# Kernel tuning notes

Hardware: AMD Instinct MI355X
Metric: run time of the kernel (lower is better)

Reference implementation:

```python
import jax, jax.numpy as jnp
import numpy as np

B, C, H, W = 16, 2048, 14, 14
D = 8192  # output_dim


def setup_inputs() -> dict:
    key = jax.random.key(0)
    k1, k2, k3, k4, k5 = jax.random.split(key, 5)
    x = jax.random.normal(k1, (B, C, H, W), dtype=jnp.float32)
    h1 = jax.random.randint(k2, (C,), 0, D, dtype=jnp.int32)
    h2 = jax.random.randint(k3, (C,), 0, D, dtype=jnp.int32)
    s1 = jax.random.randint(k4, (C,), 0, 2, dtype=jnp.int32)
    s2 = jax.random.randint(k5, (C,), 0, 2, dtype=jnp.int32)
    return {"x": x, "h1": h1, "h2": h2, "s1": s1, "s2": s2}


def _count_sketch(x_flat, h, sign, out_dim):
    # x_flat: (B, C, HW); h: (C,) hash buckets; sign: (C,) in {-1,+1}
    xs = x_flat * sign[None, :, None]
    sketch = jnp.zeros((x_flat.shape[0], out_dim, x_flat.shape[2]), dtype=x_flat.dtype)
    return sketch.at[:, h, :].add(xs)  # scatter-add over channel -> bucket


def reference(x, h1, h2, s1, s2):
    b, c, hgt, wid = x.shape
    x_flat = x.reshape(b, c, hgt * wid).astype(jnp.float32)
    sg1 = (2 * s1 - 1).astype(jnp.float32)
    sg2 = (2 * s2 - 1).astype(jnp.float32)
    sketch1 = _count_sketch(x_flat, h1, sg1, D)  # (B, D, HW)
    sketch2 = _count_sketch(x_flat, h2, sg2, D)
    fft1 = jnp.fft.fft(sketch1, axis=1)
    fft2 = jnp.fft.fft(sketch2, axis=1)
    cbp = jnp.fft.ifft(fft1 * fft2, axis=1).real  # circular conv per location
    cbp = cbp.sum(axis=-1)  # sum-pool over HW -> (B, D)
    cbp = jnp.sign(cbp) * jnp.sqrt(jnp.abs(cbp) + 1e-5)  # signed sqrt
    norm = jnp.maximum(jnp.linalg.norm(cbp, axis=1, keepdims=True), 1e-12)
    cbp = cbp / norm  # L2 normalize (matches F.normalize eps=1e-12)
    return cbp.astype(x.dtype)
```

## Files before the change

### kernel.cpp

```cpp
#include <hip/hip_runtime.h>
#include <hip/hip_bf16.h>
#include <math.h>

#define FFT_N 8192
#define HWN 196
#define CCH 2048
#define BATCH 16
#define PBLK 28
#define PPER 7

__device__ __forceinline__ int kof(int j) {
    return ((j >> 11) & 3) | (((j >> 9) & 3) << 2) | (((j >> 7) & 3) << 4) |
           (((j >> 5) & 3) << 6) | (((j >> 3) & 3) << 8) | (((j >> 1) & 3) << 10) |
           ((j & 1) << 12);
}
__device__ __forceinline__ int pof(int k) {
    return ((k & 3) << 11) | (((k >> 2) & 3) << 9) | (((k >> 4) & 3) << 7) |
           (((k >> 6) & 3) << 5) | (((k >> 8) & 3) << 3) | (((k >> 10) & 3) << 1) |
           ((k >> 12) & 1);
}

#define TW_TOTAL 1706

__device__ __forceinline__ float2 cmul(float2 a, float2 b) {
    return make_float2(a.x * b.x - a.y * b.y, a.x * b.y + a.y * b.x);
}

template <int Q4, int OFF>
__device__ __forceinline__ void pass4(float2* z, const float2* T, int tid) {
#pragma unroll
    for (int it = 0; it < FFT_N / 4 / 1024; ++it) {
        int u = tid + 1024 * it;
        int o = u & (Q4 - 1);
        int base = ((u & ~(Q4 - 1)) << 2) | o;
        float2 a = z[base], b = z[base + Q4], c = z[base + 2 * Q4], d = z[base + 3 * Q4];
        float t0r = a.x + c.x, t0i = a.y + c.y, t1r = a.x - c.x, t1i = a.y - c.y;
        float t2r = b.x + d.x, t2i = b.y + d.y, t3r = b.x - d.x, t3i = b.y - d.y;
        float2 u0 = make_float2(t0r + t2r, t0i + t2i);
        float2 u2 = make_float2(t0r - t2r, t0i - t2i);
        float2 u1 = make_float2(t1r + t3i, t1i - t3r);
        float2 u3 = make_float2(t1r - t3i, t1i + t3r);
        float2 w1;
        if constexpr (Q4 == 2048) {
            w1 = T[o & 1023];
            if (o & 1024) {
                const float r = 0.70710678118654752f;
                w1 = make_float2(r * (w1.x + w1.y), r * (w1.y - w1.x));
            }
        } else {
            w1 = T[OFF + o];
        }
        float2 w2 = make_float2(w1.x * w1.x - w1.y * w1.y, 2.f * w1.x * w1.y);
        float2 w3 = cmul(w1, w2);
        z[base] = u0;
        z[base + Q4] = cmul(u1, w1);
        z[base + 2 * Q4] = cmul(u2, w2);
        z[base + 3 * Q4] = cmul(u3, w3);
    }
    __syncthreads();
}

__device__ __forceinline__ void fft8192(float2* z, const float2* T, int tid) {
    pass4<2048, 0>(z, T, tid);
    pass4<512, 1024>(z, T, tid);
    pass4<128, 1536>(z, T, tid);
    pass4<32, 1664>(z, T, tid);
    pass4<8, 1696>(z, T, tid);
    pass4<2, 1704>(z, T, tid);
#pragma unroll
    for (int it = 0; it < 4; ++it) {
        int u = tid + 1024 * it;
        int i0 = 2 * u, i1 = 2 * u + 1;
        float2 a = z[i0], b = z[i1];
        z[i0] = make_float2(a.x + b.x, a.y + b.y);
        z[i1] = make_float2(a.x - b.x, a.y - b.y);
    }
    __syncthreads();
}

__device__ __forceinline__ void build_tables(float2* T, int tid) {
    const float w0 = -7.66990393942820573e-4f;
    {
        float s, c; sincosf(w0 * (float)tid, &s, &c); T[tid] = make_float2(c, s);
    }
    if (tid < 512) {
        float s, c; sincosf(w0 * (float)(tid * 4), &s, &c); T[1024 + tid] = make_float2(c, s);
    }
    if (tid < 128) {
        float s, c; sincosf(w0 * (float)(tid * 16), &s, &c); T[1536 + tid] = make_float2(c, s);
    }
    if (tid < 32) {
        float s, c; sincosf(w0 * (float)(tid * 64), &s, &c); T[1664 + tid] = make_float2(c, s);
    }
    if (tid < 8) {
        float s, c; sincosf(w0 * (float)(tid * 256), &s, &c); T[1696 + tid] = make_float2(c, s);
    }
    if (tid < 2) {
        float s, c; sincosf(w0 * (float)(tid * 1024), &s, &c); T[1704 + tid] = make_float2(c, s);
    }
}

__global__ __launch_bounds__(1024) void cbp_fwd(
    const float* __restrict__ x, const int* __restrict__ h1,
    const int* __restrict__ h2, const int* __restrict__ s1,
    const int* __restrict__ s2, float2* __restrict__ acc) {
    __shared__ float2 z[FFT_N];
    __shared__ float2 T[TW_TOTAL];
    int tid = threadIdx.x;
    int b = blockIdx.x / PBLK;
    int pb = blockIdx.x % PBLK;

    build_tables(T, tid);

    int c0 = tid, c1 = tid + 1024;
    int h1a = h1[c0], h2a = h2[c0], h1b = h1[c1], h2b = h2[c1];
    float g1a = (float)(2 * s1[c0] - 1), g2a = (float)(2 * s2[c0] - 1);
    float g1b = (float)(2 * s1[c1] - 1), g2b = (float)(2 * s2[c1] - 1);

    float accR[8], accI[8];
#pragma unroll
    for (int s = 0; s < 8; s++) { accR[s] = 0.f; accI[s] = 0.f; }

    const float* xa = x + (size_t)b * CCH * HWN + (size_t)c0 * HWN + pb * PPER;
    const float* xc = x + (size_t)b * CCH * HWN + (size_t)c1 * HWN + pb * PPER;

    float v0 = xa[0];
    float v1 = xc[0];

    for (int ip = 0; ip < PPER; ++ip) {
        float nv0 = 0.f, nv1 = 0.f;
        if (ip + 1 < PPER) { nv0 = xa[ip + 1]; nv1 = xc[ip + 1]; }

#pragma unroll
        for (int s = 0; s < 8; s++) z[tid + 1024 * s] = make_float2(0.f, 0.f);
        __syncthreads();
        atomicAdd(&z[h1a].x, g1a * v0);
        atomicAdd(&z[h2a].y, g2a * v0);
        atomicAdd(&z[h1b].x, g1b * v1);
        atomicAdd(&z[h2b].y, g2b * v1);
        __syncthreads();

        fft8192(z, T, tid);

#pragma unroll
        for (int s = 0; s < 8; s++) {
            int j = tid + 1024 * s;
            int k = kof(j);
            int m = (FFT_N - k) & (FFT_N - 1);
            int j2 = pof(m);
            float2 a = z[j], bz = z[j2];
            float Dr = (a.x * a.x - a.y * a.y) - (bz.x * bz.x - bz.y * bz.y);
            float Di = 2.f * (a.x * a.y + bz.x * bz.y);
            accR[s] += 0.25f * Di;
            accI[s] -= 0.25f * Dr;
        }
        __syncthreads();
        v0 = nv0; v1 = nv1;
    }

    float2* ab = acc + (size_t)b * FFT_N;
#pragma unroll
    for (int s = 0; s < 8; s++) {
        int j = tid + 1024 * s;
        atomicAdd(&ab[j].x, accR[s]);
        atomicAdd(&ab[j].y, accI[s]);
    }
}

__global__ __launch_bounds__(1024) void cbp_inv(
    const float2* __restrict__ acc, float* __restrict__ out) {
    __shared__ float2 z[FFT_N];
    __shared__ float2 T[TW_TOTAL];
    __shared__ float red[20];
    int tid = threadIdx.x;
    int b = blockIdx.x;

    build_tables(T, tid);

    const float2* ab = acc + (size_t)b * FFT_N;
#pragma unroll
    for (int s = 0; s < 8; s++) {
        int j = tid + 1024 * s;
        float2 v = ab[j];
        z[kof(j)] = make_float2(v.x, -v.y);
    }
    __syncthreads();

    fft8192(z, T, tid);

    float sv[8];
    float ss = 0.f;
#pragma unroll
    for (int s = 0; s < 8; s++) {
        int j = tid + 1024 * s;
        float v = z[j].x * (1.f / (float)FFT_N);
        float r = copysignf(sqrtf(fabsf(v) + 1e-5f), v);
        sv[s] = r;
        ss += r * r;
    }
#pragma unroll
    for (int m = 32; m >= 1; m >>= 1) ss += __shfl_xor(ss, m);
    int wave = tid >> 6, lane = tid & 63;
    if (lane == 0) red[wave] = ss;
    __syncthreads();
    if (tid == 0) {
        float tot = 0.f;
        for (int w = 0; w < 16; w++) tot += red[w];
        red[16] = fmaxf(sqrtf(tot), 1e-12f);
    }
    __syncthreads();
    float inv = 1.f / red[16];
    float* ob = out + (size_t)b * FFT_N;
#pragma unroll
    for (int s = 0; s < 8; s++) {
        int j = tid + 1024 * s;
        ob[kof(j)] = sv[s] * inv;
    }
}

extern "C" void kernel_launch(void* const* d_in, const int* in_sizes, int n_in,
                              void* d_out, int out_size, void* d_ws, size_t ws_size,
                              hipStream_t stream) {
    const float* x = (const float*)d_in[0];
    const int* h1 = (const int*)d_in[1];
    const int* h2 = (const int*)d_in[2];
    const int* s1 = (const int*)d_in[3];
    const int* s2 = (const int*)d_in[4];
    float* out = (float*)d_out;
    float2* acc = (float2*)d_ws;

    hipMemsetAsync(acc, 0, (size_t)BATCH * FFT_N * sizeof(float2), stream);
    cbp_fwd<<<BATCH * PBLK, 1024, 0, stream>>>(x, h1, h2, s1, s2, acc);
    cbp_inv<<<BATCH, 1024, 0, stream>>>(acc, (float*)out);
}
```

Measured before the change: 346.1 us.

## Process two spatial positions per FFT pass with padded LDS layout

Each block now handles 14 positions instead of 7 and runs two 8192-point FFTs together per iteration. The two FFTs share twiddle loads and barriers, and x is read as float2 pairs. LDS indices are padded by one slot every 16 elements to reduce bank conflicts in the strided butterfly passes. This halves the grid to 224 blocks and doubles LDS per block to about 150KB, which may hurt occupancy and latency hiding.

```diff
diff --git a/kernel.cpp b/kernel.cpp
--- a/kernel.cpp
+++ b/kernel.cpp
@@ -6,8 +6,11 @@
 #define HWN 196
 #define CCH 2048
 #define BATCH 16
-#define PBLK 28
-#define PPER 7
+#define PBLK 14
+#define PPER 14
+
+#define ZPAD(i) ((i) + ((i) >> 4))
+#define ZSZ 8704
 
 __device__ __forceinline__ int kof(int j) {
     return ((j >> 11) & 3) | (((j >> 9) & 3) << 2) | (((j >> 7) & 3) << 4) |
@@ -26,20 +29,30 @@
     return make_float2(a.x * b.x - a.y * b.y, a.x * b.y + a.y * b.x);
 }
 
-template <int Q4, int OFF>
-__device__ __forceinline__ void pass4(float2* z, const float2* T, int tid) {
-#pragma unroll
-    for (int it = 0; it < FFT_N / 4 / 1024; ++it) {
+__device__ __forceinline__ void bf4(float2* z, int i0, int i1, int i2, int i3,
+                                    float2 w1, float2 w2, float2 w3) {
+    float2 a = z[i0], b = z[i1], c = z[i2], d = z[i3];
+    float t0r = a.x + c.x, t0i = a.y + c.y, t1r = a.x - c.x, t1i = a.y - c.y;
+    float t2r = b.x + d.x, t2i = b.y + d.y, t3r = b.x - d.x, t3i = b.y - d.y;
+    float2 u0 = make_float2(t0r + t2r, t0i + t2i);
+    float2 u2 = make_float2(t0r - t2r, t0i - t2i);
+    float2 u1 = make_float2(t1r + t3i, t1i - t3r);
+    float2 u3 = make_float2(t1r - t3i, t1i + t3r);
+    z[i0] = u0;
+    z[i1] = cmul(u1, w1);
+    z[i2] = cmul(u2, w2);
+    z[i3] = cmul(u3, w3);
+}
+
+template <int Q4, int OFF, bool DUAL>
+__device__ __forceinline__ void pass4(float2* z0, float2* z1, const float2* T, int tid) {
+#pragma unroll
+    for (int it = 0; it < 2; ++it) {
         int u = tid + 1024 * it;
         int o = u & (Q4 - 1);
         int base = ((u & ~(Q4 - 1)) << 2) | o;
-        float2 a = z[base], b = z[base + Q4], c = z[base + 2 * Q4], d = z[base + 3 * Q4];
-        float t0r = a.x + c.x, t0i = a.y + c.y, t1r = a.x - c.x, t1i = a.y - c.y;
-        float t2r = b.x + d.x, t2i = b.y + d.y, t3r = b.x - d.x, t3i = b.y - d.y;
-        float2 u0 = make_float2(t0r + t2r, t0i + t2i);
-        float2 u2 = make_float2(t0r - t2r, t0i - t2i);
-        float2 u1 = make_float2(t1r + t3i, t1i - t3r);
-        float2 u3 = make_float2(t1r - t3i, t1i + t3r);
+        int i0 = ZPAD(base), i1 = ZPAD(base + Q4);
+        int i2 = ZPAD(base + 2 * Q4), i3 = ZPAD(base + 3 * Q4);
         float2 w1;
         if constexpr (Q4 == 2048) {
             w1 = T[o & 1023];
@@ -52,28 +65,32 @@
         }
         float2 w2 = make_float2(w1.x * w1.x - w1.y * w1.y, 2.f * w1.x * w1.y);
         float2 w3 = cmul(w1, w2);
-        z[base] = u0;
-        z[base + Q4] = cmul(u1, w1);
-        z[base + 2 * Q4] = cmul(u2, w2);
-        z[base + 3 * Q4] = cmul(u3, w3);
-    }
-    __syncthreads();
-}
-
-__device__ __forceinline__ void fft8192(float2* z, const float2* T, int tid) {
-    pass4<2048, 0>(z, T, tid);
-    pass4<512, 1024>(z, T, tid);
-    pass4<128, 1536>(z, T, tid);
-    pass4<32, 1664>(z, T, tid);
-    pass4<8, 1696>(z, T, tid);
-    pass4<2, 1704>(z, T, tid);
+        bf4(z0, i0, i1, i2, i3, w1, w2, w3);
+        if constexpr (DUAL) bf4(z1, i0, i1, i2, i3, w1, w2, w3);
+    }
+    __syncthreads();
+}
+
+template <bool DUAL>
+__device__ __forceinline__ void fft8192d(float2* z0, float2* z1, const float2* T, int tid) {
+    pass4<2048, 0, DUAL>(z0, z1, T, tid);
+    pass4<512, 1024, DUAL>(z0, z1, T, tid);
+    pass4<128, 1536, DUAL>(z0, z1, T, tid);
+    pass4<32, 1664, DUAL>(z0, z1, T, tid);
+    pass4<8, 1696, DUAL>(z0, z1, T, tid);
+    pass4<2, 1704, DUAL>(z0, z1, T, tid);
 #pragma unroll
     for (int it = 0; it < 4; ++it) {
         int u = tid + 1024 * it;
-        int i0 = 2 * u, i1 = 2 * u + 1;
-        float2 a = z[i0], b = z[i1];
-        z[i0] = make_float2(a.x + b.x, a.y + b.y);
-        z[i1] = make_float2(a.x - b.x, a.y - b.y);
+        int i0 = ZPAD(2 * u), i1 = ZPAD(2 * u + 1);
+        float2 a = z0[i0], b = z0[i1];
+        z0[i0] = make_float2(a.x + b.x, a.y + b.y);
+        z0[i1] = make_float2(a.x - b.x, a.y - b.y);
+        if constexpr (DUAL) {
+            float2 c = z1[i0], d = z1[i1];
+            z1[i0] = make_float2(c.x + d.x, c.y + d.y);
+            z1[i1] = make_float2(c.x - d.x, c.y - d.y);
+        }
     }
     __syncthreads();
 }
@@ -104,7 +121,7 @@
     const float* __restrict__ x, const int* __restrict__ h1,
     const int* __restrict__ h2, const int* __restrict__ s1,
     const int* __restrict__ s2, float2* __restrict__ acc) {
-    __shared__ float2 z[FFT_N];
+    __shared__ float2 zs[2][ZSZ];
     __shared__ float2 T[TW_TOTAL];
     int tid = threadIdx.x;
     int b = blockIdx.x / PBLK;
@@ -113,7 +130,8 @@
     build_tables(T, tid);
 
     int c0 = tid, c1 = tid + 1024;
-    int h1a = h1[c0], h2a = h2[c0], h1b = h1[c1], h2b = h2[c1];
+    int h1a = ZPAD(h1[c0]), h2a = ZPAD(h2[c0]);
+    int h1b = ZPAD(h1[c1]), h2b = ZPAD(h2[c1]);
     float g1a = (float)(2 * s1[c0] - 1), g2a = (float)(2 * s2[c0] - 1);
     float g1b = (float)(2 * s1[c1] - 1), g2b = (float)(2 * s2[c1] - 1);
 
@@ -121,26 +139,35 @@
 #pragma unroll
     for (int s = 0; s < 8; s++) { accR[s] = 0.f; accI[s] = 0.f; }
 
-    const float* xa = x + (size_t)b * CCH * HWN + (size_t)c0 * HWN + pb * PPER;
-    const float* xc = x + (size_t)b * CCH * HWN + (size_t)c1 * HWN + pb * PPER;
-
-    float v0 = xa[0];
-    float v1 = xc[0];
-
-    for (int ip = 0; ip < PPER; ++ip) {
-        float nv0 = 0.f, nv1 = 0.f;
-        if (ip + 1 < PPER) { nv0 = xa[ip + 1]; nv1 = xc[ip + 1]; }
-
-#pragma unroll
-        for (int s = 0; s < 8; s++) z[tid + 1024 * s] = make_float2(0.f, 0.f);
+    const float2* pA = (const float2*)(x + ((size_t)b * CCH + c0) * HWN + pb * PPER);
+    const float2* pB = (const float2*)(x + ((size_t)b * CCH + c1) * HWN + pb * PPER);
+
+    float2 va = pA[0];
+    float2 vb = pB[0];
+
+    float2* z0 = zs[0];
+    float2* z1 = zs[1];
+    float* zf = (float*)zs;
+
+    for (int ii = 0; ii < PPER / 2; ++ii) {
+        float2 nva = make_float2(0.f, 0.f), nvb = make_float2(0.f, 0.f);
+        if (ii + 1 < PPER / 2) { nva = pA[ii + 1]; nvb = pB[ii + 1]; }
+
+#pragma unroll
+        for (int i = 0; i < 34; ++i) zf[tid + 1024 * i] = 0.f;
         __syncthreads();
-        atomicAdd(&z[h1a].x, g1a * v0);
-        atomicAdd(&z[h2a].y, g2a * v0);
-        atomicAdd(&z[h1b].x, g1b * v1);
-        atomicAdd(&z[h2b].y, g2b * v1);
+
+        atomicAdd(&z0[h1a].x, g1a * va.x);
+        atomicAdd(&z0[h2a].y, g2a * va.x);
+        atomicAdd(&z0[h1b].x, g1b * vb.x);
+        atomicAdd(&z0[h2b].y, g2b * vb.x);
+        atomicAdd(&z1[h1a].x, g1a * va.y);
+        atomicAdd(&z1[h2a].y, g2a * va.y);
+        atomicAdd(&z1[h1b].x, g1b * vb.y);
+        atomicAdd(&z1[h2b].y, g2b * vb.y);
         __syncthreads();
 
-        fft8192(z, T, tid);
+        fft8192d<true>(z0, z1, T, tid);
 
 #pragma unroll
         for (int s = 0; s < 8; s++) {
@@ -148,14 +175,18 @@
             int k = kof(j);
             int m = (FFT_N - k) & (FFT_N - 1);
             int j2 = pof(m);
-            float2 a = z[j], bz = z[j2];
-            float Dr = (a.x * a.x - a.y * a.y) - (bz.x * bz.x - bz.y * bz.y);
-            float Di = 2.f * (a.x * a.y + bz.x * bz.y);
+            int pj = ZPAD(j), pj2 = ZPAD(j2);
+            float2 a0 = z0[pj], b0 = z0[pj2];
+            float2 a1 = z1[pj], b1 = z1[pj2];
+            float Dr = (a0.x * a0.x - a0.y * a0.y) - (b0.x * b0.x - b0.y * b0.y)
+                     + (a1.x * a1.x - a1.y * a1.y) - (b1.x * b1.x - b1.y * b1.y);
+            float Di = 2.f * (a0.x * a0.y + b0.x * b0.y)
+                     + 2.f * (a1.x * a1.y + b1.x * b1.y);
             accR[s] += 0.25f * Di;
             accI[s] -= 0.25f * Dr;
         }
         __syncthreads();
-        v0 = nv0; v1 = nv1;
+        va = nva; vb = nvb;
     }
 
     float2* ab = acc + (size_t)b * FFT_N;
@@ -169,7 +200,7 @@
 
 __global__ __launch_bounds__(1024) void cbp_inv(
     const float2* __restrict__ acc, float* __restrict__ out) {
-    __shared__ float2 z[FFT_N];
+    __shared__ float2 z[ZSZ];
     __shared__ float2 T[TW_TOTAL];
     __shared__ float red[20];
     int tid = threadIdx.x;
@@ -182,18 +213,18 @@
     for (int s = 0; s < 8; s++) {
         int j = tid + 1024 * s;
         float2 v = ab[j];
-        z[kof(j)] = make_float2(v.x, -v.y);
-    }
-    __syncthreads();
-
-    fft8192(z, T, tid);
+        z[ZPAD(kof(j))] = make_float2(v.x, -v.y);
+    }
+    __syncthreads();
+
+    fft8192d<false>(z, z, T, tid);
 
     float sv[8];
     float ss = 0.f;
 #pragma unroll
     for (int s = 0; s < 8; s++) {
         int j = tid + 1024 * s;
-        float v = z[j].x * (1.f / (float)FFT_N);
+        float v = z[ZPAD(j)].x * (1.f / (float)FFT_N);
         float r = copysignf(sqrtf(fabsf(v) + 1e-5f), v);
         sv[s] = r;
         ss += r * r;
```

Measured after the change: 314.3 us. 9.2% less time.
